# Optimization experiments

Hardware: AMD Instinct MI355X
Metric: run time of the kernel (lower is better)

Reference implementation:

```python
import jax, jax.numpy as jnp
import numpy as np

OUT_FEATURES = 4096
IN_FEATURES = 4096
GROUP_SIZE = 16


def setup_inputs() -> dict:
    key = jax.random.key(0)
    k1, k2, k3, k4 = jax.random.split(key, 4)
    n_groups = OUT_FEATURES * IN_FEATURES // GROUP_SIZE
    x = jax.random.normal(k1, (8, 2048, IN_FEATURES), dtype=jnp.float32)
    weight_q = jax.random.randint(k2, (n_groups, GROUP_SIZE), 0, 16, dtype=jnp.int32).astype(jnp.int8)
    weight_norm = jax.random.uniform(k3, (n_groups, 1), dtype=jnp.float32).astype(jnp.float16)
    bias = jax.random.normal(k4, (OUT_FEATURES,), dtype=jnp.float32)
    return {"x": x, "weight_q": weight_q, "weight_norm": weight_norm, "bias": bias}


def reference(x, weight_q, weight_norm, bias):
    # block dequant: (q/15) * per-group scale, then reshape to [out, in]
    w = (weight_q.astype(jnp.float32) / 15.0) * weight_norm.astype(jnp.float32)
    w = w.reshape(OUT_FEATURES, IN_FEATURES)
    # F.linear: x @ w^T + bias
    return jnp.einsum('bsi,oi->bso', x, w) + bias
```

## Files before the change

kernel.cpp:

```cpp
#include <hip/hip_runtime.h>

#define MDIM 16384
#define NDIM 4096
#define KDIM 4096
#define NT   64

typedef unsigned short u16;
typedef unsigned int   u32;
typedef __attribute__((ext_vector_type(8))) short bh8;
typedef __attribute__((ext_vector_type(4))) float f32x4;
typedef __attribute__((ext_vector_type(4))) int   i32x4;

__device__ __forceinline__ u16 f2bf(float f) {
  u32 u = __builtin_bit_cast(u32, f);
  u = (u + 0x7fffu + ((u >> 16) & 1u)) >> 16;
  return (u16)u;
}

__device__ __forceinline__ void gld16(const void* g, const void* lds) {
  __builtin_amdgcn_global_load_lds((const __attribute__((address_space(1))) u32*)g,
                                   (__attribute__((address_space(3))) u32*)lds, 16, 0, 0);
}

__global__ void cvt_x(const float* __restrict__ x, u16* __restrict__ xb) {
  size_t i = ((size_t)blockIdx.x * 256 + threadIdx.x) * 8;
  f32x4 a = *(const f32x4*)(x + i);
  f32x4 b = *(const f32x4*)(x + i + 4);
  bh8 o;
  o[0] = (short)f2bf(a[0]); o[1] = (short)f2bf(a[1]);
  o[2] = (short)f2bf(a[2]); o[3] = (short)f2bf(a[3]);
  o[4] = (short)f2bf(b[0]); o[5] = (short)f2bf(b[1]);
  o[6] = (short)f2bf(b[2]); o[7] = (short)f2bf(b[3]);
  *(bh8*)(xb + i) = o;
}

__global__ void deq_w(const int* __restrict__ qi, const void* __restrict__ nrm,
                      u16* __restrict__ wb) {
  __shared__ int s_q8, s_n32;
  if (threadIdx.x == 0) {
    int packed = 0;
    for (int t = 0; t < 64; ++t) { unsigned v = (unsigned)qi[t]; if (v > 15u) packed = 1; }
    int n32 = 0;
    const u16* h = (const u16*)nrm;
    for (int t = 0; t < 64; ++t) { u16 b = h[t]; if (b < 0x8000u && b > 0x3C00u) n32 = 1; }
    s_q8 = packed; s_n32 = n32;
  }
  __syncthreads();
  const bool q8 = (s_q8 != 0), n32 = (s_n32 != 0);

  int g = blockIdx.x * 256 + threadIdx.x;
  float s;
  if (n32) s = ((const float*)nrm)[g] * (1.0f / 15.0f);
  else {
    u16 hb = ((const u16*)nrm)[g];
    s = (float)__builtin_bit_cast(_Float16, hb) * (1.0f / 15.0f);
  }
  float q[16];
  if (q8) {
    i32x4 v = *(const i32x4*)((const unsigned char*)qi + (size_t)g * 16);
#pragma unroll
    for (int k = 0; k < 4; ++k) {
      int word = v[k];
      q[k*4+0] = (float)(word & 255);        q[k*4+1] = (float)((word >> 8) & 255);
      q[k*4+2] = (float)((word >> 16) & 255); q[k*4+3] = (float)((word >> 24) & 255);
    }
  } else {
    const i32x4* p = (const i32x4*)(qi + (size_t)g * 16);
#pragma unroll
    for (int k = 0; k < 4; ++k) {
      i32x4 v = p[k];
      q[k*4+0] = (float)v[0]; q[k*4+1] = (float)v[1];
      q[k*4+2] = (float)v[2]; q[k*4+3] = (float)v[3];
    }
  }
  bh8 o0, o1;
#pragma unroll
  for (int j = 0; j < 8; ++j) o0[j] = (short)f2bf(q[j] * s);
#pragma unroll
  for (int j = 0; j < 8; ++j) o1[j] = (short)f2bf(q[8 + j] * s);
  *(bh8*)(wb + (size_t)g * 16) = o0;
  *(bh8*)(wb + (size_t)g * 16 + 8) = o1;
}

__global__ __launch_bounds__(512, 2) void gemm8(const u16* __restrict__ A,
                                                const u16* __restrict__ B,
                                                const float* __restrict__ bias,
                                                float* __restrict__ out) {
  __shared__ u16 lds[65536];
  const int tid = threadIdx.x;
  const int w = tid >> 6, l = tid & 63;
  const int wm = w >> 2, wn = w & 3;

  int bid = blockIdx.x;
  int wg = (bid & 7) * 128 + (bid >> 3);
  const int bm = wg >> 4;
  const int bn = wg & 15;

  const int cs8  = ((l & 7) ^ (l >> 3)) * 8;
  const u16* aSrc = A + (size_t)(bm * 256 + w * 32 + (l >> 3)) * 4096 + cs8;
  const u16* bSrc = B + (size_t)(bn * 256 + w * 32 + (l >> 3)) * 4096 + cs8;

  const int fr  = (l & 15) * 64;
  const int sz0 = (((l >> 4)) ^ (l & 7)) * 8;
  const int sz1 = ((4 + (l >> 4)) ^ (l & 7)) * 8;

  f32x4 acc[8][4];
#pragma unroll
  for (int mi = 0; mi < 8; ++mi)
#pragma unroll
    for (int ni = 0; ni < 4; ++ni) acc[mi][ni] = (f32x4){0.f, 0.f, 0.f, 0.f};

  bh8 af[4][2], b0f[2][2], b1f[2][2];

  auto STG = [&](int op, int h, int kt) {
    const u16* s = (op ? bSrc : aSrc) + h * 65536 + kt * 64;
    int d = (op ? 32768 : 0) + ((kt & 1) * 2 + h) * 8192 + w * 1024;
    gld16(s,         &lds[d]);
    gld16(s + 32768, &lds[d + 512]);
  };
  auto RDA = [&](int buf, int mp) {
#pragma unroll
    for (int q = 0; q < 4; ++q) {
      int base = (buf * 2 + mp) * 8192 + (wm * 4 + q) * 1024 + fr;
      af[q][0] = *(const bh8*)&lds[base + sz0];
      af[q][1] = *(const bh8*)&lds[base + sz1];
    }
  };
  auto RDB = [&](int buf, int np, bh8 (&bb)[2][2]) {
#pragma unroll
    for (int q = 0; q < 2; ++q) {
      int base = 32768 + (buf * 2 + np) * 8192 + (wn * 2 + q) * 1024 + fr;
      bb[q][0] = *(const bh8*)&lds[base + sz0];
      bb[q][1] = *(const bh8*)&lds[base + sz1];
    }
  };
  auto MM = [&](int mp, int np, bh8 (&bb)[2][2]) {
    __builtin_amdgcn_s_setprio(1);
#pragma unroll
    for (int q = 0; q < 4; ++q)
#pragma unroll
      for (int r = 0; r < 2; ++r)
#pragma unroll
        for (int kk = 0; kk < 2; ++kk)
          acc[q*2+mp][r*2+np] = __builtin_amdgcn_mfma_f32_16x16x32_bf16(
              af[q][kk], bb[r][kk], acc[q*2+mp][r*2+np], 0, 0, 0);
    __builtin_amdgcn_s_setprio(0);
  };

#define PH(BUF, MP, NP, BB, RA, RB, PRE) \
  do { \
    if (RA) RDA(BUF, MP); \
    if (RB) RDB(BUF, NP, BB); \
    PRE \
    __builtin_amdgcn_s_barrier(); \
    asm volatile("s_waitcnt lgkmcnt(0)"); \
    __builtin_amdgcn_sched_barrier(0); \
    MM(MP, NP, BB); \
    __builtin_amdgcn_s_barrier(); \
  } while (0)

  STG(0, 0, 0); STG(1, 0, 0);
  STG(0, 1, 0); STG(1, 1, 0);
  STG(0, 0, 1); STG(1, 0, 1);
  asm volatile("s_waitcnt vmcnt(4)");
  __builtin_amdgcn_s_barrier();

#pragma unroll 1
  for (int i = 0; i < NT / 2 - 1; ++i) {
    const int t1 = 2 * i + 1, t2 = 2 * i + 2, t3 = 2 * i + 3;
    PH(0, 0, 0, b0f, 1, 1, { STG(0, 1, t1); });
    PH(0, 0, 1, b1f, 0, 1, { STG(1, 1, t1); });
    PH(0, 1, 0, b0f, 1, 0, { STG(0, 0, t2); });
    PH(0, 1, 1, b1f, 0, 0, { STG(1, 0, t2); asm volatile("s_waitcnt vmcnt(4)"); });
    PH(1, 0, 0, b0f, 1, 1, { STG(0, 1, t2); });
    PH(1, 0, 1, b1f, 0, 1, { STG(1, 1, t2); });
    PH(1, 1, 0, b0f, 1, 0, { STG(0, 0, t3); });
    PH(1, 1, 1, b1f, 0, 0, { STG(1, 0, t3); asm volatile("s_waitcnt vmcnt(4)"); });
  }
  PH(0, 0, 0, b0f, 1, 1, { STG(0, 1, 63); });
  PH(0, 0, 1, b1f, 0, 1, { STG(1, 1, 63); });
  PH(0, 1, 0, b0f, 1, 0, {});
  PH(0, 1, 1, b1f, 0, 0, { asm volatile("s_waitcnt vmcnt(0)"); });
  PH(1, 0, 0, b0f, 1, 1, {});
  PH(1, 0, 1, b1f, 0, 1, {});
  PH(1, 1, 0, b0f, 1, 0, {});
  PH(1, 1, 1, b1f, 0, 0, {});
#undef PH

  const int col0 = bn * 256 + wn * 64 + (l & 15);
  const int row0 = bm * 256 + wm * 128 + (l >> 4) * 4;
#pragma unroll
  for (int ni = 0; ni < 4; ++ni) {
    float bv = bias[col0 + ni * 16];
#pragma unroll
    for (int mi = 0; mi < 8; ++mi) {
      size_t base = (size_t)(row0 + mi * 16) * 4096 + (size_t)(col0 + ni * 16);
#pragma unroll
      for (int rr = 0; rr < 4; ++rr)
        out[base + (size_t)rr * 4096] = acc[mi][ni][rr] + bv;
    }
  }
}

__global__ __launch_bounds__(512, 2) void gemm_fb(const float* __restrict__ Af32,
                                                  const u16* __restrict__ Wbf,
                                                  const float* __restrict__ bias,
                                                  float* __restrict__ out) {
  __shared__ u16 lds[65536];
  const int tid = threadIdx.x;
  const int w = tid >> 6, l = tid & 63;
  const int wm = w >> 2, wn = w & 3;
  int bid = blockIdx.x;
  int wg = (bid & 7) * 128 + (bid >> 3);
  const int bm = wg >> 4, bn = wg & 15;

  int srcOffB[4], srcOffA32[4], dstSwzA[4];
#pragma unroll
  for (int j = 0; j < 4; ++j) {
    int ci = (w * 4 + j) * 64 + l;
    int r = ci >> 3, c = ci & 7;
    int cs = c ^ (r & 7);
    srcOffB[j]   = (bn * 256 + r) * 4096 + cs * 8;
    srcOffA32[j] = (bm * 256 + r) * 4096 + c * 8;
    dstSwzA[j]   = r * 64 + cs * 8;
  }
  const int ar = wm * 128 + (l & 15);
  const int br = wn * 64 + (l & 15);
  const int swz0 = (((l >> 4) + 0) ^ (l & 7)) * 8;
  const int swz1 = (((l >> 4) + 4) ^ (l & 7)) * 8;
  const int aoff0 = ar * 64 + swz0, aoff1 = ar * 64 + swz1;
  const int boff0 = 32768 + br * 64 + swz0, boff1 = 32768 + br * 64 + swz1;

  f32x4 acc[8][4];
#pragma unroll
  for (int mi = 0; mi < 8; ++mi)
#pragma unroll
    for (int ni = 0; ni < 4; ++ni) acc[mi][ni] = (f32x4){0.f, 0.f, 0.f, 0.f};

  auto STAGE = [&](int bufb, int kt) {
    const int kof = kt * 64;
#pragma unroll
    for (int j = 0; j < 4; ++j) {
      gld16(Wbf + srcOffB[j] + kof, &lds[32768 + bufb * 16384 + (w * 4 + j) * 512]);
      const float* p = Af32 + srcOffA32[j] + kof;
      f32x4 v0 = *(const f32x4*)p;
      f32x4 v1 = *(const f32x4*)(p + 4);
      bh8 o;
      o[0] = (short)f2bf(v0[0]); o[1] = (short)f2bf(v0[1]);
      o[2] = (short)f2bf(v0[2]); o[3] = (short)f2bf(v0[3]);
      o[4] = (short)f2bf(v1[0]); o[5] = (short)f2bf(v1[1]);
      o[6] = (short)f2bf(v1[2]); o[7] = (short)f2bf(v1[3]);
      *(bh8*)&lds[bufb * 16384 + dstSwzA[j]] = o;
    }
  };
  auto COMPUTE = [&](int bufb) {
    const int ab = bufb * 16384;
#pragma unroll
    for (int kk = 0; kk < 2; ++kk) {
      const int ao = ab + (kk ? aoff1 : aoff0);
      const int bo = ab + (kk ? boff1 : boff0);
      bh8 afr[8], bfr[4];
#pragma unroll
      for (int mi = 0; mi < 8; ++mi) afr[mi] = *(const bh8*)&lds[ao + mi * 1024];
#pragma unroll
      for (int ni = 0; ni < 4; ++ni) bfr[ni] = *(const bh8*)&lds[bo + ni * 1024];
#pragma unroll
      for (int mi = 0; mi < 8; ++mi)
#pragma unroll
        for (int ni = 0; ni < 4; ++ni)
          acc[mi][ni] = __builtin_amdgcn_mfma_f32_16x16x32_bf16(afr[mi], bfr[ni],
                                                                acc[mi][ni], 0, 0, 0);
    }
  };

  int buf = 0;
  STAGE(0, 0);
  __syncthreads();
  for (int kt = 0; kt < NT - 1; ++kt) {
    STAGE(buf ^ 1, kt + 1);
    COMPUTE(buf);
    __syncthreads();
    buf ^= 1;
  }
  COMPUTE(buf);

  const int col0 = bn * 256 + wn * 64 + (l & 15);
  const int row0 = bm * 256 + wm * 128 + (l >> 4) * 4;
#pragma unroll
  for (int ni = 0; ni < 4; ++ni) {
    float bv = bias[col0 + ni * 16];
#pragma unroll
    for (int mi = 0; mi < 8; ++mi) {
      size_t base = (size_t)(row0 + mi * 16) * 4096 + (size_t)(col0 + ni * 16);
#pragma unroll
      for (int rr = 0; rr < 4; ++rr)
        out[base + (size_t)rr * 4096] = acc[mi][ni][rr] + bv;
    }
  }
}

extern "C" void kernel_launch(void* const* d_in, const int* in_sizes, int n_in,
                              void* d_out, int out_size, void* d_ws, size_t ws_size,
                              hipStream_t stream) {
  const float* x    = (const float*)d_in[0];
  const int*   wq   = (const int*)d_in[1];
  const void*  wn   = d_in[2];
  const float* bias = (const float*)d_in[3];
  float*       out  = (float*)d_out;

  const size_t needA = (size_t)MDIM * KDIM * 2;
  const size_t needW = (size_t)NDIM * KDIM * 2;

  if (ws_size >= needA + needW) {
    u16* xbf = (u16*)d_ws;
    u16* wbf = (u16*)((char*)d_ws + needA);
    cvt_x<<<dim3(32768), dim3(256), 0, stream>>>(x, xbf);
    deq_w<<<dim3(4096), dim3(256), 0, stream>>>(wq, wn, wbf);
    gemm8<<<dim3(1024), dim3(512), 0, stream>>>(xbf, wbf, bias, out);
  } else if (ws_size >= needW) {
    u16* wbf = (u16*)d_ws;
    deq_w<<<dim3(4096), dim3(256), 0, stream>>>(wq, wn, wbf);
    gemm_fb<<<dim3(1024), dim3(512), 0, stream>>>(x, wbf, bias, out);
  }
}
```

Baseline: 545.1 us.

## Prefetch next phase LDS fragments into double-buffered registers during MFMA

Splits the A fragment registers into two sets and restructures each phase so the LDS reads for the next phase are issued after the barrier and overlap the current MFMA block. The explicit lgkmcnt(0) wait before the MFMAs is removed, so LDS latency is meant to be hidden behind matrix math rather than exposed at every phase. This raises VGPR pressure (an extra 8 bh8 A fragments) and depends on the compiler inserting the correct waits for the prefetched registers, which could reduce occupancy or add stalls.

After: 954.8 us. +75.2%, slower.

```diff
diff --git a/kernel.cpp b/kernel.cpp
--- a/kernel.cpp
+++ b/kernel.cpp
@@ -110,7 +110,8 @@
 #pragma unroll
     for (int ni = 0; ni < 4; ++ni) acc[mi][ni] = (f32x4){0.f, 0.f, 0.f, 0.f};
 
-  bh8 af[4][2], b0f[2][2], b1f[2][2];
+  bh8 aA[4][2], aB[4][2];
+  bh8 b0f[2][2], b1f[2][2];
 
   auto STG = [&](int op, int h, int kt) {
     const u16* s = (op ? bSrc : aSrc) + h * 65536 + kt * 64;
@@ -118,12 +119,12 @@
     gld16(s,         &lds[d]);
     gld16(s + 32768, &lds[d + 512]);
   };
-  auto RDA = [&](int buf, int mp) {
+  auto RDA = [&](int buf, int mp, bh8 (&aa)[4][2]) {
 #pragma unroll
     for (int q = 0; q < 4; ++q) {
       int base = (buf * 2 + mp) * 8192 + (wm * 4 + q) * 1024 + fr;
-      af[q][0] = *(const bh8*)&lds[base + sz0];
-      af[q][1] = *(const bh8*)&lds[base + sz1];
+      aa[q][0] = *(const bh8*)&lds[base + sz0];
+      aa[q][1] = *(const bh8*)&lds[base + sz1];
     }
   };
   auto RDB = [&](int buf, int np, bh8 (&bb)[2][2]) {
@@ -134,7 +135,7 @@
       bb[q][1] = *(const bh8*)&lds[base + sz1];
     }
   };
-  auto MM = [&](int mp, int np, bh8 (&bb)[2][2]) {
+  auto MM = [&](int mp, int np, bh8 (&aa)[4][2], bh8 (&bb)[2][2]) {
     __builtin_amdgcn_s_setprio(1);
 #pragma unroll
     for (int q = 0; q < 4; ++q)
@@ -143,48 +144,52 @@
 #pragma unroll
         for (int kk = 0; kk < 2; ++kk)
           acc[q*2+mp][r*2+np] = __builtin_amdgcn_mfma_f32_16x16x32_bf16(
-              af[q][kk], bb[r][kk], acc[q*2+mp][r*2+np], 0, 0, 0);
+              aa[q][kk], bb[r][kk], acc[q*2+mp][r*2+np], 0, 0, 0);
     __builtin_amdgcn_s_setprio(0);
   };
 
-#define PH(BUF, MP, NP, BB, RA, RB, PRE) \
+#define PH(MP, NP, AA, BB, RDAHEAD, PRE) \
   do { \
-    if (RA) RDA(BUF, MP); \
-    if (RB) RDB(BUF, NP, BB); \
     PRE \
     __builtin_amdgcn_s_barrier(); \
-    asm volatile("s_waitcnt lgkmcnt(0)"); \
+    asm volatile("" ::: "memory"); \
+    RDAHEAD \
     __builtin_amdgcn_sched_barrier(0); \
-    MM(MP, NP, BB); \
+    MM(MP, NP, AA, BB); \
+    asm volatile("" ::: "memory"); \
     __builtin_amdgcn_s_barrier(); \
   } while (0)
 
-  STG(0, 0, 0); STG(1, 0, 0);
-  STG(0, 1, 0); STG(1, 1, 0);
+  STG(0, 0, 0); STG(1, 0, 0); STG(0, 1, 0); STG(1, 1, 0);
   STG(0, 0, 1); STG(1, 0, 1);
   asm volatile("s_waitcnt vmcnt(4)");
   __builtin_amdgcn_s_barrier();
+  asm volatile("" ::: "memory");
+  RDA(0, 0, aA); RDB(0, 0, b0f);
 
 #pragma unroll 1
   for (int i = 0; i < NT / 2 - 1; ++i) {
-    const int t1 = 2 * i + 1, t2 = 2 * i + 2, t3 = 2 * i + 3;
-    PH(0, 0, 0, b0f, 1, 1, { STG(0, 1, t1); });
-    PH(0, 0, 1, b1f, 0, 1, { STG(1, 1, t1); });
-    PH(0, 1, 0, b0f, 1, 0, { STG(0, 0, t2); });
-    PH(0, 1, 1, b1f, 0, 0, { STG(1, 0, t2); asm volatile("s_waitcnt vmcnt(4)"); });
-    PH(1, 0, 0, b0f, 1, 1, { STG(0, 1, t2); });
-    PH(1, 0, 1, b1f, 0, 1, { STG(1, 1, t2); });
-    PH(1, 1, 0, b0f, 1, 0, { STG(0, 0, t3); });
-    PH(1, 1, 1, b1f, 0, 0, { STG(1, 0, t3); asm volatile("s_waitcnt vmcnt(4)"); });
-  }
-  PH(0, 0, 0, b0f, 1, 1, { STG(0, 1, 63); });
-  PH(0, 0, 1, b1f, 0, 1, { STG(1, 1, 63); });
-  PH(0, 1, 0, b0f, 1, 0, {});
-  PH(0, 1, 1, b1f, 0, 0, { asm volatile("s_waitcnt vmcnt(0)"); });
-  PH(1, 0, 0, b0f, 1, 1, {});
-  PH(1, 0, 1, b1f, 0, 1, {});
-  PH(1, 1, 0, b0f, 1, 0, {});
-  PH(1, 1, 1, b1f, 0, 0, {});
+    const int tb = 2 * i + 1, tc = 2 * i + 2, td = 2 * i + 3;
+    PH(0, 0, aA, b0f, { RDB(0, 1, b1f); },                   { STG(0, 1, tb); });
+    PH(0, 1, aA, b1f, { RDA(0, 1, aB); },                    { STG(1, 1, tb); });
+    PH(1, 0, aB, b0f, { },                                   { STG(0, 0, tc); });
+    PH(1, 1, aB, b1f, { RDA(1, 0, aA); RDB(1, 0, b0f); },
+       { STG(1, 0, tc); asm volatile("s_waitcnt vmcnt(4)"); });
+    PH(0, 0, aA, b0f, { RDB(1, 1, b1f); },                   { STG(0, 1, tc); });
+    PH(0, 1, aA, b1f, { RDA(1, 1, aB); },                    { STG(1, 1, tc); });
+    PH(1, 0, aB, b0f, { },                                   { STG(0, 0, td); });
+    PH(1, 1, aB, b1f, { RDA(0, 0, aA); RDB(0, 0, b0f); },
+       { STG(1, 0, td); asm volatile("s_waitcnt vmcnt(4)"); });
+  }
+  PH(0, 0, aA, b0f, { RDB(0, 1, b1f); },                     { STG(0, 1, 63); });
+  PH(0, 1, aA, b1f, { RDA(0, 1, aB); },                      { STG(1, 1, 63); });
+  PH(1, 0, aB, b0f, { },                                     { });
+  PH(1, 1, aB, b1f, { RDA(1, 0, aA); RDB(1, 0, b0f); },
+     { asm volatile("s_waitcnt vmcnt(0)"); });
+  PH(0, 0, aA, b0f, { RDB(1, 1, b1f); },                     { });
+  PH(0, 1, aA, b1f, { RDA(1, 1, aB); },                      { });
+  PH(1, 0, aB, b0f, { },                                     { });
+  PH(1, 1, aB, b1f, { },                                     { });
 #undef PH
 
   const int col0 = bn * 256 + wn * 64 + (l & 15);
```

## Replace 8-wave phased GEMM with 16-wave double-buffered GEMM

Applied to the files above, without the earlier changes.

Switches the main bf16 GEMM from 512 threads (8 waves, 128x64 warp tiles, an 8-phase interleaved LDS read/MFMA schedule with priority hints) to 1024 threads (16 waves, 64x64 warp tiles) using a simple two-buffer load/compute loop. The intent is to hide latency through more waves per block instead of a hand-tuned software pipeline. In exchange it gives up the phased overlap and setprio scheduling and reduces register reuse per wave. The launch bound of 4 blocks of 1024 threads is likely unattainable, and LDS traffic per MFMA goes up.

New measurement: 882.8 us. 61.9% more time.

```diff
diff --git a/kernel.cpp b/kernel.cpp
--- a/kernel.cpp
+++ b/kernel.cpp
@@ -82,10 +82,10 @@
   *(bh8*)(wb + (size_t)g * 16 + 8) = o1;
 }
 
-__global__ __launch_bounds__(512, 2) void gemm8(const u16* __restrict__ A,
-                                                const u16* __restrict__ B,
-                                                const float* __restrict__ bias,
-                                                float* __restrict__ out) {
+__global__ __launch_bounds__(1024, 4) void gemm16(const u16* __restrict__ A,
+                                                  const u16* __restrict__ B,
+                                                  const float* __restrict__ bias,
+                                                  float* __restrict__ out) {
   __shared__ u16 lds[65536];
   const int tid = threadIdx.x;
   const int w = tid >> 6, l = tid & 63;
@@ -96,104 +96,87 @@
   const int bm = wg >> 4;
   const int bn = wg & 15;
 
-  const int cs8  = ((l & 7) ^ (l >> 3)) * 8;
-  const u16* aSrc = A + (size_t)(bm * 256 + w * 32 + (l >> 3)) * 4096 + cs8;
-  const u16* bSrc = B + (size_t)(bn * 256 + w * 32 + (l >> 3)) * 4096 + cs8;
-
-  const int fr  = (l & 15) * 64;
-  const int sz0 = (((l >> 4)) ^ (l & 7)) * 8;
-  const int sz1 = ((4 + (l >> 4)) ^ (l & 7)) * 8;
-
-  f32x4 acc[8][4];
-#pragma unroll
-  for (int mi = 0; mi < 8; ++mi)
+  const int cs8   = ((l & 7) ^ (l >> 3)) * 8;
+  const int srow  = (w >> 1) * 32 + (w & 1) * 8 + (l >> 3);
+  const u16* aS0 = A + (size_t)(bm * 256 + srow) * 4096 + cs8;
+  const u16* aS1 = A + (size_t)(bm * 256 + 16 + srow) * 4096 + cs8;
+  const u16* bS0 = B + (size_t)(bn * 256 + srow) * 4096 + cs8;
+  const u16* bS1 = B + (size_t)(bn * 256 + 16 + srow) * 4096 + cs8;
+  const int dstW = w * 512;
+
+  const int rl  = (l & 15) * 64;
+  const int ck0 = ((l >> 4) ^ (l & 7)) * 8;
+  const int ck1 = ((4 + (l >> 4)) ^ (l & 7)) * 8;
+
+  f32x4 acc[4][4];
+#pragma unroll
+  for (int mi = 0; mi < 4; ++mi)
 #pragma unroll
     for (int ni = 0; ni < 4; ++ni) acc[mi][ni] = (f32x4){0.f, 0.f, 0.f, 0.f};
 
-  bh8 af[4][2], b0f[2][2], b1f[2][2];
-
-  auto STG = [&](int op, int h, int kt) {
-    const u16* s = (op ? bSrc : aSrc) + h * 65536 + kt * 64;
-    int d = (op ? 32768 : 0) + ((kt & 1) * 2 + h) * 8192 + w * 1024;
-    gld16(s,         &lds[d]);
-    gld16(s + 32768, &lds[d + 512]);
+  auto STG = [&](int buf, int kt) {
+    const int k = kt * 64;
+    gld16(aS0 + k, &lds[(buf * 2 + 0) * 8192 + dstW]);
+    gld16(aS1 + k, &lds[(buf * 2 + 1) * 8192 + dstW]);
+    gld16(bS0 + k, &lds[32768 + (buf * 2 + 0) * 8192 + dstW]);
+    gld16(bS1 + k, &lds[32768 + (buf * 2 + 1) * 8192 + dstW]);
   };
-  auto RDA = [&](int buf, int mp) {
-#pragma unroll
-    for (int q = 0; q < 4; ++q) {
-      int base = (buf * 2 + mp) * 8192 + (wm * 4 + q) * 1024 + fr;
-      af[q][0] = *(const bh8*)&lds[base + sz0];
-      af[q][1] = *(const bh8*)&lds[base + sz1];
+
+  auto COMPUTE = [&](int buf) {
+#pragma unroll
+    for (int kk = 0; kk < 2; ++kk) {
+      const int ck = kk ? ck1 : ck0;
+      bh8 af[4], bf[4];
+#pragma unroll
+      for (int mi = 0; mi < 4; ++mi) {
+        const int G = wm * 4 + mi;
+        af[mi] = *(const bh8*)&lds[(buf * 2 + (G & 1)) * 8192 + (G >> 1) * 1024 + rl + ck];
+      }
+#pragma unroll
+      for (int ni = 0; ni < 4; ++ni) {
+        const int G = wn * 4 + ni;
+        bf[ni] = *(const bh8*)&lds[32768 + (buf * 2 + (G & 1)) * 8192 + (G >> 1) * 1024 + rl + ck];
+      }
+#pragma unroll
+      for (int mi = 0; mi < 4; ++mi)
+#pragma unroll
+        for (int ni = 0; ni < 4; ++ni)
+          acc[mi][ni] = __builtin_amdgcn_mfma_f32_16x16x32_bf16(af[mi], bf[ni],
+                                                                acc[mi][ni], 0, 0, 0);
     }
   };
-  auto RDB = [&](int buf, int np, bh8 (&bb)[2][2]) {
-#pragma unroll
-    for (int q = 0; q < 2; ++q) {
-      int base = 32768 + (buf * 2 + np) * 8192 + (wn * 2 + q) * 1024 + fr;
-      bb[q][0] = *(const bh8*)&lds[base + sz0];
-      bb[q][1] = *(const bh8*)&lds[base + sz1];
-    }
-  };
-  auto MM = [&](int mp, int np, bh8 (&bb)[2][2]) {
-    __builtin_amdgcn_s_setprio(1);
-#pragma unroll
-    for (int q = 0; q < 4; ++q)
-#pragma unroll
-      for (int r = 0; r < 2; ++r)
-#pragma unroll
-        for (int kk = 0; kk < 2; ++kk)
-          acc[q*2+mp][r*2+np] = __builtin_amdgcn_mfma_f32_16x16x32_bf16(
-              af[q][kk], bb[r][kk], acc[q*2+mp][r*2+np], 0, 0, 0);
-    __builtin_amdgcn_s_setprio(0);
-  };
-
-#define PH(BUF, MP, NP, BB, RA, RB, PRE) \
-  do { \
-    if (RA) RDA(BUF, MP); \
-    if (RB) RDB(BUF, NP, BB); \
-    PRE \
-    __builtin_amdgcn_s_barrier(); \
-    asm volatile("s_waitcnt lgkmcnt(0)"); \
-    __builtin_amdgcn_sched_barrier(0); \
-    MM(MP, NP, BB); \
-    __builtin_amdgcn_s_barrier(); \
-  } while (0)
-
-  STG(0, 0, 0); STG(1, 0, 0);
-  STG(0, 1, 0); STG(1, 1, 0);
-  STG(0, 0, 1); STG(1, 0, 1);
-  asm volatile("s_waitcnt vmcnt(4)");
-  __builtin_amdgcn_s_barrier();
-
+
+#define BAR asm volatile("" ::: "memory"); __builtin_amdgcn_s_barrier(); \
+            asm volatile("" ::: "memory");
+
+  STG(0, 0);
 #pragma unroll 1
-  for (int i = 0; i < NT / 2 - 1; ++i) {
-    const int t1 = 2 * i + 1, t2 = 2 * i + 2, t3 = 2 * i + 3;
-    PH(0, 0, 0, b0f, 1, 1, { STG(0, 1, t1); });
-    PH(0, 0, 1, b1f, 0, 1, { STG(1, 1, t1); });
-    PH(0, 1, 0, b0f, 1, 0, { STG(0, 0, t2); });
-    PH(0, 1, 1, b1f, 0, 0, { STG(1, 0, t2); asm volatile("s_waitcnt vmcnt(4)"); });
-    PH(1, 0, 0, b0f, 1, 1, { STG(0, 1, t2); });
-    PH(1, 0, 1, b1f, 0, 1, { STG(1, 1, t2); });
-    PH(1, 1, 0, b0f, 1, 0, { STG(0, 0, t3); });
-    PH(1, 1, 1, b1f, 0, 0, { STG(1, 0, t3); asm volatile("s_waitcnt vmcnt(4)"); });
-  }
-  PH(0, 0, 0, b0f, 1, 1, { STG(0, 1, 63); });
-  PH(0, 0, 1, b1f, 0, 1, { STG(1, 1, 63); });
-  PH(0, 1, 0, b0f, 1, 0, {});
-  PH(0, 1, 1, b1f, 0, 0, { asm volatile("s_waitcnt vmcnt(0)"); });
-  PH(1, 0, 0, b0f, 1, 1, {});
-  PH(1, 0, 1, b1f, 0, 1, {});
-  PH(1, 1, 0, b0f, 1, 0, {});
-  PH(1, 1, 1, b1f, 0, 0, {});
-#undef PH
+  for (int i = 0; i < NT / 2; ++i) {
+    const int a = 2 * i;
+    STG(1, a + 1);
+    asm volatile("s_waitcnt vmcnt(4)");
+    BAR;
+    COMPUTE(0);
+    BAR;
+    if (a + 2 < NT) {
+      STG(0, a + 2);
+      asm volatile("s_waitcnt vmcnt(4)");
+    } else {
+      asm volatile("s_waitcnt vmcnt(0)");
+    }
+    BAR;
+    COMPUTE(1);
+    BAR;
+  }
+#undef BAR
 
   const int col0 = bn * 256 + wn * 64 + (l & 15);
-  const int row0 = bm * 256 + wm * 128 + (l >> 4) * 4;
+  const int row0 = bm * 256 + wm * 64 + (l >> 4) * 4;
 #pragma unroll
   for (int ni = 0; ni < 4; ++ni) {
     float bv = bias[col0 + ni * 16];
 #pragma unroll
-    for (int mi = 0; mi < 8; ++mi) {
+    for (int mi = 0; mi < 4; ++mi) {
       size_t base = (size_t)(row0 + mi * 16) * 4096 + (size_t)(col0 + ni * 16);
 #pragma unroll
       for (int rr = 0; rr < 4; ++rr)
@@ -316,7 +299,7 @@
     u16* wbf = (u16*)((char*)d_ws + needA);
     cvt_x<<<dim3(32768), dim3(256), 0, stream>>>(x, xbf);
     deq_w<<<dim3(4096), dim3(256), 0, stream>>>(wq, wn, wbf);
-    gemm8<<<dim3(1024), dim3(512), 0, stream>>>(xbf, wbf, bias, out);
+    gemm16<<<dim3(1024), dim3(1024), 0, stream>>>(xbf, wbf, bias, out);
   } else if (ws_size >= needW) {
     u16* wbf = (u16*)d_ws;
     deq_w<<<dim3(4096), dim3(256), 0, stream>>>(wq, wn, wbf);
```
